# Kernel tuning notes

Hardware: AMD Instinct MI355X
Metric: run time of the kernel (lower is better)

## Reference

```python
import jax, jax.numpy as jnp
import numpy as np
import math

B, S, D = 8, 1024, 1024
H, R = 16, 8
HD = D // H
SCALING = 16.0 / R  # alpha / rank = 2.0
DFF = 4 * D
DC = D // 2
NC = 3


def setup_inputs() -> dict:
    key = jax.random.key(0)
    ks = jax.random.split(key, 32)
    n = lambda i, shape, s=0.02: jax.random.normal(ks[i], shape, dtype=jnp.float32) * s
    inp = {
        'hidden_states': jax.random.normal(ks[0], (B, S, D), dtype=jnp.float32),
        # LoRA-adapted projections: base weight W [out,in], lora_A [r,in], lora_B [out,r]
        'Wq': n(1, (D, D)), 'Aq': n(2, (R, D), 0.1), 'Bq': n(3, (D, R), 0.02),
        'Wk': n(4, (D, D)), 'Ak': n(5, (R, D), 0.1), 'Bk': n(6, (D, R), 0.02),
        'Wv': n(7, (D, D)), 'Av': n(8, (R, D), 0.1), 'Bv': n(9, (D, R), 0.02),
        'Wo': n(10, (D, D)), 'Ao': n(11, (R, D), 0.1), 'Bo': n(12, (D, R), 0.02),
        'ln1_g': jnp.ones((D,), jnp.float32), 'ln1_b': jnp.zeros((D,), jnp.float32),
        'ln2_g': jnp.ones((D,), jnp.float32), 'ln2_b': jnp.zeros((D,), jnp.float32),
        'W1': n(13, (DFF, D)), 'b1': jnp.zeros((DFF,), jnp.float32),
        'W2': n(14, (D, DFF)), 'b2': jnp.zeros((D,), jnp.float32),
        'Wc1': n(15, (DC, D)), 'bc1': jnp.zeros((DC,), jnp.float32),
        'Wc2': n(16, (NC, DC)), 'bc2': jnp.zeros((NC,), jnp.float32),
    }
    return inp


def _lora_linear(x, W, A, Bm):
    # F.linear(x, W) + scaling * F.linear(F.linear(x, A), B)
    return x @ W.T + SCALING * ((x @ A.T) @ Bm.T)


def _layer_norm(x, g, b, eps=1e-5):
    mu = jnp.mean(x, axis=-1, keepdims=True)
    var = jnp.var(x, axis=-1, keepdims=True)
    return (x - mu) * jax.lax.rsqrt(var + eps) * g + b


def reference(hidden_states, Wq, Aq, Bq, Wk, Ak, Bk, Wv, Av, Bv, Wo, Ao, Bo,
              ln1_g, ln1_b, ln2_g, ln2_b, W1, b1, W2, b2, Wc1, bc1, Wc2, bc2):
    residual = hidden_states
    h = _layer_norm(hidden_states, ln1_g, ln1_b)
    # attention
    q = _lora_linear(h, Wq, Aq, Bq).reshape(B, S, H, HD).transpose(0, 2, 1, 3)
    k = _lora_linear(h, Wk, Ak, Bk).reshape(B, S, H, HD).transpose(0, 2, 1, 3)
    v = _lora_linear(h, Wv, Av, Bv).reshape(B, S, H, HD).transpose(0, 2, 1, 3)
    scores = jnp.einsum('bhqd,bhkd->bhqk', q, k) / math.sqrt(HD)
    probs = jax.nn.softmax(scores, axis=-1)
    ctx = jnp.einsum('bhqk,bhkd->bhqd', probs, v)
    ctx = ctx.transpose(0, 2, 1, 3).reshape(B, S, D)
    attn_out = _lora_linear(ctx, Wo, Ao, Bo)
    h = residual + attn_out
    residual = h
    hn = _layer_norm(h, ln2_g, ln2_b)
    ffn = jax.nn.gelu(hn @ W1.T + b1, approximate=False) @ W2.T + b2
    h = residual + ffn
    pooled = h[:, 0]  # [B, D]
    logits = jax.nn.gelu(pooled @ Wc1.T + bc1, approximate=False) @ Wc2.T + bc2
    return logits
```

## Files before the change

### kernel.cpp

```cpp
#include <hip/hip_runtime.h>
#include <hip/hip_bf16.h>


__device__ __forceinline__ float blo(unsigned int u) {
  union { unsigned int i; float f; } v; v.i = u << 16; return v.f;
}
__device__ __forceinline__ float bhi(unsigned int u) {
  union { unsigned int i; float f; } v; v.i = u & 0xffff0000u; return v.f;
}
__device__ __forceinline__ unsigned short f2bf(float f) {
  union { float f; unsigned int i; } v; v.f = f;
  unsigned int u = v.i;
  u += 0x7FFFu + ((u >> 16) & 1u);
  return (unsigned short)(u >> 16);
}
__device__ __forceinline__ float gelu_exact(float x) {
  return 0.5f * x * (1.0f + erff(x * 0.70710678118654752440f));
}
__device__ __forceinline__ float wave_sum(float v) {
#pragma unroll
  for (int o = 1; o < 64; o <<= 1) v += __shfl_xor(v, o);
  return v;
}

__global__ __launch_bounds__(256) void ln_fused(
    const float* __restrict__ x, const float* __restrict__ g,
    const float* __restrict__ b, unsigned short* __restrict__ hbf,
    float* __restrict__ x0) {
  int blk = blockIdx.x;
  int f32out = (blk >= 8192);
  const float* xr = f32out ? (x + (size_t)(blk - 8192) * 1048576)
                           : (x + (size_t)blk * 1024);
  int t = threadIdx.x;
  float4 v = ((const float4*)xr)[t];
  float s  = v.x + v.y + v.z + v.w;
  float sq = v.x * v.x + v.y * v.y + v.z * v.z + v.w * v.w;
#pragma unroll
  for (int o = 32; o; o >>= 1) { s += __shfl_down(s, o); sq += __shfl_down(sq, o); }
  __shared__ float rs_[4], rq_[4], stat[2];
  int w = t >> 6, l = t & 63;
  if (l == 0) { rs_[w] = s; rq_[w] = sq; }
  __syncthreads();
  if (t == 0) {
    float S = rs_[0] + rs_[1] + rs_[2] + rs_[3];
    float Q = rq_[0] + rq_[1] + rq_[2] + rq_[3];
    float mu = S * (1.0f / 1024.0f);
    float var = Q * (1.0f / 1024.0f) - mu * mu;
    stat[0] = mu; stat[1] = rsqrtf(var + 1e-5f);
  }
  __syncthreads();
  float mu = stat[0], rstd = stat[1];
  float4 gg = ((const float4*)g)[t];
  float4 bb = ((const float4*)b)[t];
  float o0 = (v.x - mu) * rstd * gg.x + bb.x;
  float o1 = (v.y - mu) * rstd * gg.y + bb.y;
  float o2 = (v.z - mu) * rstd * gg.z + bb.z;
  float o3 = (v.w - mu) * rstd * gg.w + bb.w;
  if (f32out) {
    float* op = x0 + (size_t)(blk - 8192) * 1024 + t * 4;
    op[0] = o0; op[1] = o1; op[2] = o2; op[3] = o3;
  } else {
    unsigned short* op = hbf + (size_t)blk * 1024 + t * 4;
    op[0] = f2bf(o0); op[1] = f2bf(o1); op[2] = f2bf(o2); op[3] = f2bf(o3);
  }
}

template <int CPW>
__global__ __launch_bounds__(256) void skinny_gemm(
    const float* __restrict__ X, long xrs, long xhs,
    const float* __restrict__ W, const float* __restrict__ bias,
    const float* __restrict__ Amat, const float* __restrict__ Bmat,
    const float* __restrict__ resid, long rstride,
    float* __restrict__ Y, int N, int K, int do_gelu) {
  __shared__ float sX[8][1024];
  __shared__ float sT[8][8][4];
  __shared__ float T[8][8];
  int t = threadIdx.x, w = t >> 6, l = t & 63;
  int bcol = blockIdx.x * (4 * CPW);
  int col0 = bcol + w * CPW;
  int head = bcol >> 6;
  const float* Xb = X + (size_t)head * xhs;
  float acc[CPW][8];
#pragma unroll
  for (int c = 0; c < CPW; ++c)
#pragma unroll
    for (int m = 0; m < 8; ++m) acc[c][m] = 0.f;
  for (int kc = 0; kc < K; kc += 1024) {
    for (int i = t; i < 2048; i += 256) {
      int m = i >> 8, p = i & 255;
      ((float4*)sX[m])[p] = *(const float4*)(Xb + (size_t)m * xrs + kc + p * 4);
    }
    __syncthreads();
    if (Amat && kc == 0) {
      int m = t >> 5, r = (t >> 2) & 7, q = t & 3;
      float s = 0.f;
      const float* ar = Amat + r * 1024 + q * 256;
      const float* xr = &sX[m][q * 256];
      for (int j = 0; j < 256; j += 4)
        s += xr[j] * ar[j] + xr[j+1] * ar[j+1] + xr[j+2] * ar[j+2] + xr[j+3] * ar[j+3];
      sT[m][r][q] = s;
      __syncthreads();
      if (t < 64) {
        int mm = t >> 3, rr = t & 7;
        T[mm][rr] = sT[mm][rr][0] + sT[mm][rr][1] + sT[mm][rr][2] + sT[mm][rr][3];
      }
      __syncthreads();
    }
#pragma unroll
    for (int i = 0; i < 4; ++i) {
      int k = i * 256 + l * 4;
      float4 xv[8];
#pragma unroll
      for (int m = 0; m < 8; ++m) xv[m] = *(const float4*)&sX[m][k];
#pragma unroll
      for (int c = 0; c < CPW; ++c) {
        float4 wv = *(const float4*)(W + (size_t)(col0 + c) * K + kc + k);
#pragma unroll
        for (int m = 0; m < 8; ++m)
          acc[c][m] += wv.x * xv[m].x + wv.y * xv[m].y + wv.z * xv[m].z + wv.w * xv[m].w;
      }
    }
    __syncthreads();
  }
#pragma unroll
  for (int c = 0; c < CPW; ++c)
#pragma unroll
    for (int m = 0; m < 8; ++m) {
      float v = acc[c][m];
#pragma unroll
      for (int o = 32; o; o >>= 1) v += __shfl_down(v, o);
      acc[c][m] = v;
    }
  if (l == 0) {
#pragma unroll
    for (int c = 0; c < CPW; ++c) {
      int col = col0 + c;
      float bv = bias ? bias[col] : 0.f;
      float lb[8];
      if (Amat) {
#pragma unroll
        for (int r = 0; r < 8; ++r) lb[r] = Bmat[col * 8 + r];
      }
#pragma unroll
      for (int m = 0; m < 8; ++m) {
        float v = acc[c][m] + bv;
        if (Amat) {
#pragma unroll
          for (int r = 0; r < 8; ++r) v += 2.0f * lb[r] * T[m][r];
        }
        if (do_gelu) v = gelu_exact(v);
        if (resid) v += resid[(size_t)m * rstride + col];
        Y[(size_t)m * N + col] = v;
      }
    }
  }
}

__global__ __launch_bounds__(256) void pullback_kernel(
    const float* __restrict__ q0, const float* __restrict__ Wk,
    const float* __restrict__ Ak, const float* __restrict__ Bk,
    float* __restrict__ qh) {
  int head = blockIdx.x >> 2, cchunk = blockIdx.x & 3;
  int t = threadIdx.x;
  int c = cchunk * 256 + t;
  __shared__ float sq[8][64];
  __shared__ float sT[8][8][4];
  __shared__ float T[8][8];
  if (t < 512) { int b = t >> 6, d = t & 63; sq[b][d] = q0[b * 1024 + head * 64 + d]; }
  __syncthreads();
  {
    int b = t >> 5, r = (t >> 2) & 7, q = t & 3;
    float s = 0.f;
#pragma unroll
    for (int j = 0; j < 16; ++j) {
      int d = q * 16 + j;
      s += sq[b][d] * Bk[(head * 64 + d) * 8 + r];
    }
    sT[b][r][q] = s;
  }
  __syncthreads();
  if (t < 64) {
    int b = t >> 3, r = t & 7;
    T[b][r] = sT[b][r][0] + sT[b][r][1] + sT[b][r][2] + sT[b][r][3];
  }
  __syncthreads();
  float acc[8] = {0.f, 0.f, 0.f, 0.f, 0.f, 0.f, 0.f, 0.f};
#pragma unroll 4
  for (int d = 0; d < 64; ++d) {
    float wv = Wk[(size_t)(head * 64 + d) * 1024 + c];
#pragma unroll
    for (int b = 0; b < 8; ++b) acc[b] += sq[b][d] * wv;
  }
  float av[8];
#pragma unroll
  for (int r = 0; r < 8; ++r) av[r] = Ak[r * 1024 + c];
#pragma unroll
  for (int b = 0; b < 8; ++b) {
    float v = acc[b];
#pragma unroll
    for (int r = 0; r < 8; ++r) v += 2.0f * T[b][r] * av[r];
    qh[(size_t)(head * 8 + b) * 1024 + c] = v;
  }
}

__global__ __launch_bounds__(512) void attn_flash(
    const float* __restrict__ qh, const unsigned short* __restrict__ hbf,
    float* __restrict__ opart, float* __restrict__ ml) {
  int b = blockIdx.x & 7, kc = blockIdx.x >> 3;
  int t = threadIdx.x, wid = t >> 6, l = t & 63;
  __shared__ float S[32][16];
  __shared__ float smax[16];
  __shared__ float pS[32][16];
  const unsigned short* hb = hbf + (size_t)b * 1048576 + (size_t)kc * 32768;
  float qv[2][16];
#pragma unroll
  for (int hi = 0; hi < 2; ++hi) {
    const float4* qp = (const float4*)(qh + (size_t)((hi * 8 + wid) * 8 + b) * 1024 + l * 16);
#pragma unroll
    for (int i = 0; i < 4; ++i) {
      float4 q4 = qp[i];
      qv[hi][i * 4 + 0] = q4.x; qv[hi][i * 4 + 1] = q4.y;
      qv[hi][i * 4 + 2] = q4.z; qv[hi][i * 4 + 3] = q4.w;
    }
  }
  for (int k = 0; k < 32; ++k) {
    const uint4* hp = (const uint4*)(hb + (size_t)k * 1024 + l * 16);
    uint4 u0 = hp[0], u1 = hp[1];
    float hv[16];
    hv[0]=blo(u0.x); hv[1]=bhi(u0.x); hv[2]=blo(u0.y); hv[3]=bhi(u0.y);
    hv[4]=blo(u0.z); hv[5]=bhi(u0.z); hv[6]=blo(u0.w); hv[7]=bhi(u0.w);
    hv[8]=blo(u1.x); hv[9]=bhi(u1.x); hv[10]=blo(u1.y); hv[11]=bhi(u1.y);
    hv[12]=blo(u1.z); hv[13]=bhi(u1.z); hv[14]=blo(u1.w); hv[15]=bhi(u1.w);
    float s0 = 0.f, s1 = 0.f;
#pragma unroll
    for (int j = 0; j < 16; ++j) { s0 += qv[0][j] * hv[j]; s1 += qv[1][j] * hv[j]; }
    s0 = wave_sum(s0); s1 = wave_sum(s1);
    if (l == 0) {
      S[k][wid]     = s0 * 0.125f;
      S[k][wid + 8] = s1 * 0.125f;
    }
  }
  __syncthreads();
  if (t < 16) {
    float m = -1e30f;
    for (int k = 0; k < 32; ++k) m = fmaxf(m, S[k][t]);
    float ls = 0.f;
    for (int k = 0; k < 32; ++k) ls += expf(S[k][t] - m);
    smax[t] = m;
    ml[((size_t)(b * 32 + kc) * 16 + t) * 2]     = m;
    ml[((size_t)(b * 32 + kc) * 16 + t) * 2 + 1] = ls;
  }
  __syncthreads();
  { int k = t >> 4, h = t & 15;
    pS[k][h] = expf(S[k][h] - smax[h]); }
  __syncthreads();
  int c0 = t * 2;
  float a0[16], a1[16];
#pragma unroll
  for (int h = 0; h < 16; ++h) { a0[h] = 0.f; a1[h] = 0.f; }
  for (int k = 0; k < 32; ++k) {
    unsigned int u = *(const unsigned int*)(hb + (size_t)k * 1024 + c0);
    float h0 = blo(u), h1 = bhi(u);
    float4 p0 = *(const float4*)&pS[k][0];
    float4 p1 = *(const float4*)&pS[k][4];
    float4 p2 = *(const float4*)&pS[k][8];
    float4 p3 = *(const float4*)&pS[k][12];
    float pk[16] = {p0.x, p0.y, p0.z, p0.w, p1.x, p1.y, p1.z, p1.w,
                    p2.x, p2.y, p2.z, p2.w, p3.x, p3.y, p3.z, p3.w};
#pragma unroll
    for (int h = 0; h < 16; ++h) { a0[h] += pk[h] * h0; a1[h] += pk[h] * h1; }
  }
  float* ob = opart + ((size_t)(b * 32 + kc) * 16) * 1024 + c0;
#pragma unroll
  for (int h = 0; h < 16; ++h) {
    float2 o2; o2.x = a0[h]; o2.y = a1[h];
    *(float2*)(ob + (size_t)h * 1024) = o2;
  }
}

__global__ __launch_bounds__(256) void combine_kernel(
    const float* __restrict__ opart, const float* __restrict__ ml,
    float* __restrict__ pv) {
  int blk = blockIdx.x;
  int hh = blk >> 3, b = blk & 7;
  int t = threadIdx.x;
  __shared__ float am[32], al[32], e[32], Linv;
  if (t < 32) {
    am[t] = ml[((size_t)(b * 32 + t) * 16 + hh) * 2];
    al[t] = ml[((size_t)(b * 32 + t) * 16 + hh) * 2 + 1];
  }
  __syncthreads();
  if (t == 0) {
    float M = -1e30f;
    for (int c = 0; c < 32; ++c) M = fmaxf(M, am[c]);
    float L = 0.f;
    for (int c = 0; c < 32; ++c) {
      float ee = expf(am[c] - M);
      e[c] = ee;
      L += al[c] * ee;
    }
    Linv = 1.f / L;
  }
  __syncthreads();
  int c0 = t * 4;
  float4 a = (float4){0.f, 0.f, 0.f, 0.f};
#pragma unroll 8
  for (int kc = 0; kc < 32; ++kc) {
    float4 v = *(const float4*)(opart + ((size_t)(b * 32 + kc) * 16 + hh) * 1024 + c0);
    float ee = e[kc];
    a.x += ee * v.x; a.y += ee * v.y; a.z += ee * v.z; a.w += ee * v.w;
  }
  float inv = Linv;
  a.x *= inv; a.y *= inv; a.z *= inv; a.w *= inv;
  *(float4*)(pv + (size_t)(hh * 8 + b) * 1024 + c0) = a;
}

__global__ __launch_bounds__(256) void ln2_ffn1(
    const float* __restrict__ h2, const float* __restrict__ g,
    const float* __restrict__ bb, const float* __restrict__ W1,
    const float* __restrict__ b1, float* __restrict__ mid) {
  __shared__ float sX[8][1024];
  int t = threadIdx.x, w = t >> 6, l = t & 63;
  for (int i = t; i < 2048; i += 256)
    ((float4*)sX)[i] = ((const float4*)h2)[i];
  __syncthreads();
#pragma unroll
  for (int rr = 0; rr < 2; ++rr) {
    int r = w + rr * 4;
    float4 xv[4];
#pragma unroll
    for (int i = 0; i < 4; ++i) xv[i] = *(const float4*)&sX[r][i * 256 + l * 4];
    float s = 0.f, sq = 0.f;
#pragma unroll
    for (int i = 0; i < 4; ++i) {
      s  += xv[i].x + xv[i].y + xv[i].z + xv[i].w;
      sq += xv[i].x * xv[i].x + xv[i].y * xv[i].y + xv[i].z * xv[i].z + xv[i].w * xv[i].w;
    }
    s = wave_sum(s); sq = wave_sum(sq);
    float mu = s * (1.f / 1024.f);
    float rstd = rsqrtf(sq * (1.f / 1024.f) - mu * mu + 1e-5f);
#pragma unroll
    for (int i = 0; i < 4; ++i) {
      float4 g4 = ((const float4*)g)[i * 64 + l];
      float4 b4 = ((const float4*)bb)[i * 64 + l];
      float4 o;
      o.x = (xv[i].x - mu) * rstd * g4.x + b4.x;
      o.y = (xv[i].y - mu) * rstd * g4.y + b4.y;
      o.z = (xv[i].z - mu) * rstd * g4.z + b4.z;
      o.w = (xv[i].w - mu) * rstd * g4.w + b4.w;
      *(float4*)&sX[r][i * 256 + l * 4] = o;
    }
  }
  __syncthreads();
  int col0 = blockIdx.x * 16 + w * 4;
  float acc[4][8];
#pragma unroll
  for (int c = 0; c < 4; ++c)
#pragma unroll
    for (int m = 0; m < 8; ++m) acc[c][m] = 0.f;
#pragma unroll
  for (int i = 0; i < 4; ++i) {
    int k = i * 256 + l * 4;
    float4 xv[8];
#pragma unroll
    for (int m = 0; m < 8; ++m) xv[m] = *(const float4*)&sX[m][k];
#pragma unroll
    for (int c = 0; c < 4; ++c) {
      float4 wv = *(const float4*)(W1 + (size_t)(col0 + c) * 1024 + k);
#pragma unroll
      for (int m = 0; m < 8; ++m)
        acc[c][m] += wv.x * xv[m].x + wv.y * xv[m].y + wv.z * xv[m].z + wv.w * xv[m].w;
    }
  }
#pragma unroll
  for (int c = 0; c < 4; ++c)
#pragma unroll
    for (int m = 0; m < 8; ++m) acc[c][m] = wave_sum(acc[c][m]);
  if (l == 0) {
#pragma unroll
    for (int c = 0; c < 4; ++c) {
      int col = col0 + c;
      float bv = b1[col];
#pragma unroll
      for (int m = 0; m < 8; ++m)
        mid[(size_t)m * 4096 + col] = gelu_exact(acc[c][m] + bv);
    }
  }
}

__global__ __launch_bounds__(256) void logits_kernel(
    const float* __restrict__ cmid, const float* __restrict__ Wc2,
    const float* __restrict__ bc2, float* __restrict__ out) {
  int t = threadIdx.x;
  int o = t >> 3, s = t & 7;
  float a = 0.f;
  if (o < 24) {
    int b = o / 3, n = o % 3;
    const float* x = cmid + b * 512 + s * 64;
    const float* w = Wc2 + n * 512 + s * 64;
#pragma unroll
    for (int k = 0; k < 64; ++k) a += x[k] * w[k];
  }
  __shared__ float part[32][8];
  part[o][s] = a;
  __syncthreads();
  if (t < 24) {
    float v = bc2[t % 3];
#pragma unroll
    for (int ss = 0; ss < 8; ++ss) v += part[t][ss];
    out[t] = v;
  }
}

extern "C" void kernel_launch(void* const* d_in, const int* in_sizes, int n_in,
                              void* d_out, int out_size, void* d_ws, size_t ws_size,
                              hipStream_t stream) {
  const float* x    = (const float*)d_in[0];
  const float* Wq   = (const float*)d_in[1];
  const float* Aq   = (const float*)d_in[2];
  const float* Bq   = (const float*)d_in[3];
  const float* Wk   = (const float*)d_in[4];
  const float* Ak   = (const float*)d_in[5];
  const float* Bk   = (const float*)d_in[6];
  const float* Wv   = (const float*)d_in[7];
  const float* Av   = (const float*)d_in[8];
  const float* Bv   = (const float*)d_in[9];
  const float* Wo   = (const float*)d_in[10];
  const float* Ao   = (const float*)d_in[11];
  const float* Bo   = (const float*)d_in[12];
  const float* ln1g = (const float*)d_in[13];
  const float* ln1b = (const float*)d_in[14];
  const float* ln2g = (const float*)d_in[15];
  const float* ln2b = (const float*)d_in[16];
  const float* W1   = (const float*)d_in[17];
  const float* b1   = (const float*)d_in[18];
  const float* W2   = (const float*)d_in[19];
  const float* b2   = (const float*)d_in[20];
  const float* Wc1  = (const float*)d_in[21];
  const float* bc1  = (const float*)d_in[22];
  const float* Wc2  = (const float*)d_in[23];
  const float* bc2  = (const float*)d_in[24];

  char* ws = (char*)d_ws;
  size_t off = 0;
  auto alloc = [&](size_t bytes) {
    void* p = ws + off;
    off += (bytes + 255) & ~(size_t)255;
    return p;
  };
  unsigned short* h_bf = (unsigned short*)alloc((size_t)8192 * 1024 * 2);
  float* qh      = (float*)alloc((size_t)128 * 1024 * 4);
  float* opart   = (float*)alloc((size_t)256 * 16 * 1024 * 4);
  float* ml      = (float*)alloc((size_t)8 * 32 * 16 * 2 * 4);
  float* pvb     = (float*)alloc((size_t)128 * 1024 * 4);
  float* x0   = (float*)alloc(8 * 1024 * 4);
  float* q0   = (float*)alloc(8 * 1024 * 4);
  float* ctx0 = (float*)alloc(8 * 1024 * 4);
  float* h2   = (float*)alloc(8 * 1024 * 4);
  float* mid  = (float*)alloc(8 * 4096 * 4);
  float* pooled = (float*)alloc(8 * 1024 * 4);
  float* cmid = (float*)alloc(8 * 512 * 4);

  ln_fused<<<8200, 256, 0, stream>>>(x, ln1g, ln1b, h_bf, x0);
  skinny_gemm<1><<<256, 256, 0, stream>>>(x0, 1024, 0, Wq, nullptr, Aq, Bq,
                                          nullptr, 0, q0, 1024, 1024, 0);
  pullback_kernel<<<64, 256, 0, stream>>>(q0, Wk, Ak, Bk, qh);
  attn_flash<<<256, 512, 0, stream>>>(qh, h_bf, opart, ml);
  combine_kernel<<<128, 256, 0, stream>>>(opart, ml, pvb);
  skinny_gemm<1><<<256, 256, 0, stream>>>(pvb, 1024, 8192, Wv, nullptr, Av, Bv,
                                          nullptr, 0, ctx0, 1024, 1024, 0);
  skinny_gemm<1><<<256, 256, 0, stream>>>(ctx0, 1024, 0, Wo, nullptr, Ao, Bo,
                                          x, 1048576, h2, 1024, 1024, 0);
  ln2_ffn1<<<256, 256, 0, stream>>>(h2, ln2g, ln2b, W1, b1, mid);
  skinny_gemm<1><<<256, 256, 0, stream>>>(mid, 4096, 0, W2, b2, nullptr, nullptr,
                                          h2, 1024, pooled, 1024, 4096, 0);
  skinny_gemm<1><<<128, 256, 0, stream>>>(pooled, 1024, 0, Wc1, bc1, nullptr,
                                          nullptr, nullptr, 0, cmid, 512, 1024, 1);
  logits_kernel<<<1, 256, 0, stream>>>(cmid, Wc2, bc2, (float*)d_out);
}
```

Before: 158.1 us.

## Fuse LN1, Q projection and K pullback; fuse classifier head with atomics

Merges the layernorm, the Q LoRA projection of token 0 and the K pullback into one kernel, so 64 blocks handle Q/K while the other 8192 blocks produce the bf16 normalized hidden states. Each of the 64 blocks recomputes the same 64 Q columns for its head redundantly instead of reading a shared q0. The classifier's two layers are also merged into one 32-block kernel that accumulates logits with atomicAdd into an output pre-seeded with bc2 by ln2_ffn1. This removes three launches and two intermediate buffers, at the cost of redundant Q work and a dependence on atomic float ordering.

```diff
diff --git a/kernel.cpp b/kernel.cpp
--- a/kernel.cpp
+++ b/kernel.cpp
@@ -23,45 +23,153 @@
   return v;
 }
 
-__global__ __launch_bounds__(256) void ln_fused(
+__global__ __launch_bounds__(256) void fused_ln_qk(
     const float* __restrict__ x, const float* __restrict__ g,
-    const float* __restrict__ b, unsigned short* __restrict__ hbf,
-    float* __restrict__ x0) {
-  int blk = blockIdx.x;
-  int f32out = (blk >= 8192);
-  const float* xr = f32out ? (x + (size_t)(blk - 8192) * 1048576)
-                           : (x + (size_t)blk * 1024);
-  int t = threadIdx.x;
-  float4 v = ((const float4*)xr)[t];
-  float s  = v.x + v.y + v.z + v.w;
-  float sq = v.x * v.x + v.y * v.y + v.z * v.z + v.w * v.w;
-#pragma unroll
-  for (int o = 32; o; o >>= 1) { s += __shfl_down(s, o); sq += __shfl_down(sq, o); }
-  __shared__ float rs_[4], rq_[4], stat[2];
-  int w = t >> 6, l = t & 63;
-  if (l == 0) { rs_[w] = s; rq_[w] = sq; }
-  __syncthreads();
-  if (t == 0) {
-    float S = rs_[0] + rs_[1] + rs_[2] + rs_[3];
-    float Q = rq_[0] + rq_[1] + rq_[2] + rq_[3];
-    float mu = S * (1.0f / 1024.0f);
-    float var = Q * (1.0f / 1024.0f) - mu * mu;
-    stat[0] = mu; stat[1] = rsqrtf(var + 1e-5f);
-  }
-  __syncthreads();
-  float mu = stat[0], rstd = stat[1];
-  float4 gg = ((const float4*)g)[t];
-  float4 bb = ((const float4*)b)[t];
-  float o0 = (v.x - mu) * rstd * gg.x + bb.x;
-  float o1 = (v.y - mu) * rstd * gg.y + bb.y;
-  float o2 = (v.z - mu) * rstd * gg.z + bb.z;
-  float o3 = (v.w - mu) * rstd * gg.w + bb.w;
-  if (f32out) {
-    float* op = x0 + (size_t)(blk - 8192) * 1024 + t * 4;
-    op[0] = o0; op[1] = o1; op[2] = o2; op[3] = o3;
-  } else {
-    unsigned short* op = hbf + (size_t)blk * 1024 + t * 4;
-    op[0] = f2bf(o0); op[1] = f2bf(o1); op[2] = f2bf(o2); op[3] = f2bf(o3);
+    const float* __restrict__ b, const float* __restrict__ Wq,
+    const float* __restrict__ Aq, const float* __restrict__ Bq,
+    const float* __restrict__ Wk, const float* __restrict__ Ak,
+    const float* __restrict__ Bk, unsigned short* __restrict__ hbf,
+    float* __restrict__ qh) {
+  int bid = blockIdx.x;
+  int t = threadIdx.x, w = t >> 6, l = t & 63;
+
+  if (bid >= 64) {
+    int row = bid - 64;
+    const float* xr = x + (size_t)row * 1024;
+    float4 v = ((const float4*)xr)[t];
+    float s  = v.x + v.y + v.z + v.w;
+    float sq = v.x * v.x + v.y * v.y + v.z * v.z + v.w * v.w;
+#pragma unroll
+    for (int o = 32; o; o >>= 1) { s += __shfl_down(s, o); sq += __shfl_down(sq, o); }
+    __shared__ float rs_[4], rq_[4], stat[2];
+    if (l == 0) { rs_[w] = s; rq_[w] = sq; }
+    __syncthreads();
+    if (t == 0) {
+      float S = rs_[0] + rs_[1] + rs_[2] + rs_[3];
+      float Q = rq_[0] + rq_[1] + rq_[2] + rq_[3];
+      float mu = S * (1.0f / 1024.0f);
+      float var = Q * (1.0f / 1024.0f) - mu * mu;
+      stat[0] = mu; stat[1] = rsqrtf(var + 1e-5f);
+    }
+    __syncthreads();
+    float mu = stat[0], rstd = stat[1];
+    float4 gg = ((const float4*)g)[t];
+    float4 bb = ((const float4*)b)[t];
+    unsigned short* op = hbf + (size_t)row * 1024 + t * 4;
+    op[0] = f2bf((v.x - mu) * rstd * gg.x + bb.x);
+    op[1] = f2bf((v.y - mu) * rstd * gg.y + bb.y);
+    op[2] = f2bf((v.z - mu) * rstd * gg.z + bb.z);
+    op[3] = f2bf((v.w - mu) * rstd * gg.w + bb.w);
+    return;
+  }
+
+  int head = bid >> 2, cchunk = bid & 3;
+  __shared__ float sX[8][1024];
+  __shared__ float sq8[8][64];
+  __shared__ float sT[8][8][4];
+  __shared__ float Tq[8][8];
+  __shared__ float Tk[8][8];
+#pragma unroll
+  for (int rr = 0; rr < 2; ++rr) {
+    int r = w + rr * 4;
+    const float* xr = x + (size_t)r * 1048576;
+    float4 xv[4];
+#pragma unroll
+    for (int i = 0; i < 4; ++i) xv[i] = ((const float4*)xr)[i * 64 + l];
+    float s = 0.f, sqr = 0.f;
+#pragma unroll
+    for (int i = 0; i < 4; ++i) {
+      s   += xv[i].x + xv[i].y + xv[i].z + xv[i].w;
+      sqr += xv[i].x * xv[i].x + xv[i].y * xv[i].y + xv[i].z * xv[i].z + xv[i].w * xv[i].w;
+    }
+    s = wave_sum(s); sqr = wave_sum(sqr);
+    float mu = s * (1.f / 1024.f);
+    float rstd = rsqrtf(sqr * (1.f / 1024.f) - mu * mu + 1e-5f);
+#pragma unroll
+    for (int i = 0; i < 4; ++i) {
+      float4 g4 = ((const float4*)g)[i * 64 + l];
+      float4 b4 = ((const float4*)b)[i * 64 + l];
+      float4 o;
+      o.x = (xv[i].x - mu) * rstd * g4.x + b4.x;
+      o.y = (xv[i].y - mu) * rstd * g4.y + b4.y;
+      o.z = (xv[i].z - mu) * rstd * g4.z + b4.z;
+      o.w = (xv[i].w - mu) * rstd * g4.w + b4.w;
+      *(float4*)&sX[r][i * 256 + l * 4] = o;
+    }
+  }
+  __syncthreads();
+  {
+    int m = t >> 5, r = (t >> 2) & 7, q = t & 3;
+    float s = 0.f;
+    const float* ar = Aq + r * 1024 + q * 256;
+    const float* xr = &sX[m][q * 256];
+    for (int j = 0; j < 256; j += 4)
+      s += xr[j] * ar[j] + xr[j+1] * ar[j+1] + xr[j+2] * ar[j+2] + xr[j+3] * ar[j+3];
+    sT[m][r][q] = s;
+  }
+  __syncthreads();
+  if (t < 64) {
+    int m = t >> 3, r = t & 7;
+    Tq[m][r] = sT[m][r][0] + sT[m][r][1] + sT[m][r][2] + sT[m][r][3];
+  }
+  __syncthreads();
+  for (int ci = 0; ci < 16; ++ci) {
+    int d = w * 16 + ci;
+    int col = head * 64 + d;
+    float acc[8] = {0.f, 0.f, 0.f, 0.f, 0.f, 0.f, 0.f, 0.f};
+#pragma unroll
+    for (int i = 0; i < 4; ++i) {
+      int k = i * 256 + l * 4;
+      float4 wv = *(const float4*)(Wq + (size_t)col * 1024 + k);
+#pragma unroll
+      for (int m = 0; m < 8; ++m) {
+        float4 xv = *(const float4*)&sX[m][k];
+        acc[m] += wv.x * xv.x + wv.y * xv.y + wv.z * xv.z + wv.w * xv.w;
+      }
+    }
+#pragma unroll
+    for (int m = 0; m < 8; ++m) acc[m] = wave_sum(acc[m]);
+    if (l == 0) {
+#pragma unroll
+      for (int m = 0; m < 8; ++m) {
+        float v = acc[m];
+#pragma unroll
+        for (int r = 0; r < 8; ++r) v += 2.f * Bq[col * 8 + r] * Tq[m][r];
+        sq8[m][d] = v;
+      }
+    }
+  }
+  __syncthreads();
+  {
+    int bb2 = t >> 5, r = (t >> 2) & 7, q = t & 3;
+    float s = 0.f;
+#pragma unroll
+    for (int j = 0; j < 16; ++j) {
+      int d = q * 16 + j;
+      s += sq8[bb2][d] * Bk[(head * 64 + d) * 8 + r];
+    }
+    sT[bb2][r][q] = s;
+  }
+  __syncthreads();
+  if (t < 64) {
+    int bb2 = t >> 3, r = t & 7;
+    Tk[bb2][r] = sT[bb2][r][0] + sT[bb2][r][1] + sT[bb2][r][2] + sT[bb2][r][3];
+  }
+  __syncthreads();
+  int c = cchunk * 256 + t;
+  float acc[8] = {0.f, 0.f, 0.f, 0.f, 0.f, 0.f, 0.f, 0.f};
+#pragma unroll 4
+  for (int d = 0; d < 64; ++d) {
+    float wv = Wk[(size_t)(head * 64 + d) * 1024 + c];
+#pragma unroll
+    for (int bb2 = 0; bb2 < 8; ++bb2) acc[bb2] += sq8[bb2][d] * wv;
+  }
+#pragma unroll
+  for (int bb2 = 0; bb2 < 8; ++bb2) {
+    float v = acc[bb2];
+#pragma unroll
+    for (int r = 0; r < 8; ++r) v += 2.f * Tk[bb2][r] * Ak[r * 1024 + c];
+    qh[(size_t)(head * 8 + bb2) * 1024 + c] = v;
   }
 }
 
@@ -156,53 +264,6 @@
   }
 }
 
-__global__ __launch_bounds__(256) void pullback_kernel(
-    const float* __restrict__ q0, const float* __restrict__ Wk,
-    const float* __restrict__ Ak, const float* __restrict__ Bk,
-    float* __restrict__ qh) {
-  int head = blockIdx.x >> 2, cchunk = blockIdx.x & 3;
-  int t = threadIdx.x;
-  int c = cchunk * 256 + t;
-  __shared__ float sq[8][64];
-  __shared__ float sT[8][8][4];
-  __shared__ float T[8][8];
-  if (t < 512) { int b = t >> 6, d = t & 63; sq[b][d] = q0[b * 1024 + head * 64 + d]; }
-  __syncthreads();
-  {
-    int b = t >> 5, r = (t >> 2) & 7, q = t & 3;
-    float s = 0.f;
-#pragma unroll
-    for (int j = 0; j < 16; ++j) {
-      int d = q * 16 + j;
-      s += sq[b][d] * Bk[(head * 64 + d) * 8 + r];
-    }
-    sT[b][r][q] = s;
-  }
-  __syncthreads();
-  if (t < 64) {
-    int b = t >> 3, r = t & 7;
-    T[b][r] = sT[b][r][0] + sT[b][r][1] + sT[b][r][2] + sT[b][r][3];
-  }
-  __syncthreads();
-  float acc[8] = {0.f, 0.f, 0.f, 0.f, 0.f, 0.f, 0.f, 0.f};
-#pragma unroll 4
-  for (int d = 0; d < 64; ++d) {
-    float wv = Wk[(size_t)(head * 64 + d) * 1024 + c];
-#pragma unroll
-    for (int b = 0; b < 8; ++b) acc[b] += sq[b][d] * wv;
-  }
-  float av[8];
-#pragma unroll
-  for (int r = 0; r < 8; ++r) av[r] = Ak[r * 1024 + c];
-#pragma unroll
-  for (int b = 0; b < 8; ++b) {
-    float v = acc[b];
-#pragma unroll
-    for (int r = 0; r < 8; ++r) v += 2.0f * T[b][r] * av[r];
-    qh[(size_t)(head * 8 + b) * 1024 + c] = v;
-  }
-}
-
 __global__ __launch_bounds__(512) void attn_flash(
     const float* __restrict__ qh, const unsigned short* __restrict__ hbf,
     float* __restrict__ opart, float* __restrict__ ml) {
@@ -318,9 +379,11 @@
 __global__ __launch_bounds__(256) void ln2_ffn1(
     const float* __restrict__ h2, const float* __restrict__ g,
     const float* __restrict__ bb, const float* __restrict__ W1,
-    const float* __restrict__ b1, float* __restrict__ mid) {
+    const float* __restrict__ b1, float* __restrict__ mid,
+    const float* __restrict__ bc2, float* __restrict__ out) {
   __shared__ float sX[8][1024];
   int t = threadIdx.x, w = t >> 6, l = t & 63;
+  if (blockIdx.x == 0 && t < 24) out[t] = bc2[t % 3];
   for (int i = t; i < 2048; i += 256)
     ((float4*)sX)[i] = ((const float4*)h2)[i];
   __syncthreads();
@@ -388,27 +451,56 @@
   }
 }
 
-__global__ __launch_bounds__(256) void logits_kernel(
-    const float* __restrict__ cmid, const float* __restrict__ Wc2,
-    const float* __restrict__ bc2, float* __restrict__ out) {
-  int t = threadIdx.x;
-  int o = t >> 3, s = t & 7;
-  float a = 0.f;
-  if (o < 24) {
-    int b = o / 3, n = o % 3;
-    const float* x = cmid + b * 512 + s * 64;
-    const float* w = Wc2 + n * 512 + s * 64;
-#pragma unroll
-    for (int k = 0; k < 64; ++k) a += x[k] * w[k];
-  }
-  __shared__ float part[32][8];
-  part[o][s] = a;
+__global__ __launch_bounds__(256) void cls_logits(
+    const float* __restrict__ pooled, const float* __restrict__ Wc1,
+    const float* __restrict__ bc1, const float* __restrict__ Wc2,
+    float* __restrict__ out) {
+  __shared__ float sX[8][1024];
+  __shared__ float plog[4][8][3];
+  int t = threadIdx.x, w = t >> 6, l = t & 63;
+  for (int i = t; i < 2048; i += 256)
+    ((float4*)sX)[i] = ((const float4*)pooled)[i];
+  __syncthreads();
+  float preg[8][3];
+#pragma unroll
+  for (int m = 0; m < 8; ++m)
+#pragma unroll
+    for (int n = 0; n < 3; ++n) preg[m][n] = 0.f;
+  for (int ci = 0; ci < 4; ++ci) {
+    int col = blockIdx.x * 16 + w * 4 + ci;
+    float acc[8] = {0.f, 0.f, 0.f, 0.f, 0.f, 0.f, 0.f, 0.f};
+#pragma unroll
+    for (int i = 0; i < 4; ++i) {
+      int k = i * 256 + l * 4;
+      float4 wv = *(const float4*)(Wc1 + (size_t)col * 1024 + k);
+#pragma unroll
+      for (int m = 0; m < 8; ++m) {
+        float4 xv = *(const float4*)&sX[m][k];
+        acc[m] += wv.x * xv.x + wv.y * xv.y + wv.z * xv.z + wv.w * xv.w;
+      }
+    }
+#pragma unroll
+    for (int m = 0; m < 8; ++m) acc[m] = wave_sum(acc[m]);
+    if (l == 0) {
+#pragma unroll
+      for (int m = 0; m < 8; ++m) {
+        float v = gelu_exact(acc[m] + bc1[col]);
+#pragma unroll
+        for (int n = 0; n < 3; ++n) preg[m][n] += v * Wc2[n * 512 + col];
+      }
+    }
+  }
+  if (l == 0) {
+#pragma unroll
+    for (int m = 0; m < 8; ++m)
+#pragma unroll
+      for (int n = 0; n < 3; ++n) plog[w][m][n] = preg[m][n];
+  }
   __syncthreads();
   if (t < 24) {
-    float v = bc2[t % 3];
-#pragma unroll
-    for (int ss = 0; ss < 8; ++ss) v += part[t][ss];
-    out[t] = v;
+    int m = t / 3, n = t % 3;
+    float v = plog[0][m][n] + plog[1][m][n] + plog[2][m][n] + plog[3][m][n];
+    atomicAdd(&out[t], v);
   }
 }
 
@@ -453,28 +545,22 @@
   float* opart   = (float*)alloc((size_t)256 * 16 * 1024 * 4);
   float* ml      = (float*)alloc((size_t)8 * 32 * 16 * 2 * 4);
   float* pvb     = (float*)alloc((size_t)128 * 1024 * 4);
-  float* x0   = (float*)alloc(8 * 1024 * 4);
-  float* q0   = (float*)alloc(8 * 1024 * 4);
   float* ctx0 = (float*)alloc(8 * 1024 * 4);
   float* h2   = (float*)alloc(8 * 1024 * 4);
   float* mid  = (float*)alloc(8 * 4096 * 4);
   float* pooled = (float*)alloc(8 * 1024 * 4);
-  float* cmid = (float*)alloc(8 * 512 * 4);
-
-  ln_fused<<<8200, 256, 0, stream>>>(x, ln1g, ln1b, h_bf, x0);
-  skinny_gemm<1><<<256, 256, 0, stream>>>(x0, 1024, 0, Wq, nullptr, Aq, Bq,
-                                          nullptr, 0, q0, 1024, 1024, 0);
-  pullback_kernel<<<64, 256, 0, stream>>>(q0, Wk, Ak, Bk, qh);
+
+  fused_ln_qk<<<8256, 256, 0, stream>>>(x, ln1g, ln1b, Wq, Aq, Bq,
+                                        Wk, Ak, Bk, h_bf, qh);
   attn_flash<<<256, 512, 0, stream>>>(qh, h_bf, opart, ml);
   combine_kernel<<<128, 256, 0, stream>>>(opart, ml, pvb);
   skinny_gemm<1><<<256, 256, 0, stream>>>(pvb, 1024, 8192, Wv, nullptr, Av, Bv,
                                           nullptr, 0, ctx0, 1024, 1024, 0);
   skinny_gemm<1><<<256, 256, 0, stream>>>(ctx0, 1024, 0, Wo, nullptr, Ao, Bo,
                                           x, 1048576, h2, 1024, 1024, 0);
-  ln2_ffn1<<<256, 256, 0, stream>>>(h2, ln2g, ln2b, W1, b1, mid);
+  ln2_ffn1<<<256, 256, 0, stream>>>(h2, ln2g, ln2b, W1, b1, mid, bc2,
+                                    (float*)d_out);
   skinny_gemm<1><<<256, 256, 0, stream>>>(mid, 4096, 0, W2, b2, nullptr, nullptr,
                                           h2, 1024, pooled, 1024, 4096, 0);
-  skinny_gemm<1><<<128, 256, 0, stream>>>(pooled, 1024, 0, Wc1, bc1, nullptr,
-                                          nullptr, nullptr, 0, cmid, 512, 1024, 1);
-  logits_kernel<<<1, 256, 0, stream>>>(cmid, Wc2, bc2, (float*)d_out);
-}
+  cls_logits<<<32, 256, 0, stream>>>(pooled, Wc1, bc1, Wc2, (float*)d_out);
+}
```

New measurement: 164.9 us. +4.3%, slower.
